# Optimization experiments

Measured on AMD Instinct MI355X. Metric: run time of the kernel, lower is better.

The kernel has to match this reference:

```python
import jax, jax.numpy as jnp
import numpy as np

B, C, N = 4, 512, 4096
C8 = C // 8


def setup_inputs() -> dict:
    key = jax.random.key(0)
    ks = jax.random.split(key, 8)
    s = 0.05  # keep logits in a sane range for softmax
    return {
        "x": jax.random.normal(ks[0], (B, C, N), dtype=jnp.float32),
        "Wq": jax.random.normal(ks[1], (C8, C), dtype=jnp.float32) * s,
        "bq": jax.random.normal(ks[2], (C8,), dtype=jnp.float32) * s,
        "Wk": jax.random.normal(ks[3], (C8, C), dtype=jnp.float32) * s,
        "bk": jax.random.normal(ks[4], (C8,), dtype=jnp.float32) * s,
        "Wv": jax.random.normal(ks[5], (C, C), dtype=jnp.float32) * s,
        "bv": jax.random.normal(ks[6], (C,), dtype=jnp.float32) * s,
        "gamma": jax.random.normal(ks[7], (1,), dtype=jnp.float32),
    }


def reference(x, Wq, bq, Wk, bk, Wv, bv, gamma):
    # Conv1d with kernel_size=1 == per-position linear over channels.
    # x: [B, C, N]
    q = jnp.einsum('oc,bcn->bno', Wq, x) + bq               # [B, N, C8] (already permuted)
    k = jnp.einsum('oc,bcn->bon', Wk, x) + bk[None, :, None]  # [B, C8, N]
    v = jnp.einsum('oc,bcn->bon', Wv, x) + bv[None, :, None]  # [B, C, N]
    # attmap[b, i, j] = <q_i, k_j>; NOTE: no 1/sqrt(d) scaling in the original.
    att = jnp.einsum('bic,bcj->bij', q, k)                  # [B, N, N]
    score = jax.nn.softmax(att, axis=-1)                    # softmax over j
    # out = bmm(value, score.permute(0,2,1)) -> out[b,c,i] = sum_j v[b,c,j] * score[b,i,j]
    out = jnp.einsum('bcj,bij->bci', v, score)              # [B, C, N]
    return gamma * out + x
```

## Files before the change

kernel.cpp:

```cpp
#include <hip/hip_runtime.h>
#include <hip/hip_bf16.h>

typedef __hip_bfloat16 bf16;
typedef __attribute__((ext_vector_type(8))) short short8;
typedef __attribute__((ext_vector_type(4))) float fl4;

#define Bn 4
#define Cn 512
#define C8n 64
#define Nn 4096
#define XKS 536

union BfU { bf16 h; unsigned short u; };
__device__ __forceinline__ unsigned short f2b(float f) { BfU c; c.h = __float2bfloat16(f); return c.u; }
__device__ __forceinline__ float b2f_(unsigned short u) { BfU c; c.u = u; return __bfloat162float(c.h); }

#define MFMA16(a, b, c) __builtin_amdgcn_mfma_f32_16x16x32_bf16(a, b, c, 0, 0, 0)
#define ROR1(x) __uint_as_float(__builtin_amdgcn_update_dpp(0, (int)__float_as_uint(x), 0x121, 0xF, 0xF, true))
#define ROR2(x) __uint_as_float(__builtin_amdgcn_update_dpp(0, (int)__float_as_uint(x), 0x122, 0xF, 0xF, true))
#define ROR4(x) __uint_as_float(__builtin_amdgcn_update_dpp(0, (int)__float_as_uint(x), 0x124, 0xF, 0xF, true))
#define ROR8(x) __uint_as_float(__builtin_amdgcn_update_dpp(0, (int)__float_as_uint(x), 0x128, 0xF, 0xF, true))

__global__ __launch_bounds__(128) void prep_w(
    const float* __restrict__ Wq, const float* __restrict__ bq,
    const float* __restrict__ Wk, const float* __restrict__ bk,
    const float* __restrict__ Wv, const float* __restrict__ bv,
    bf16* __restrict__ whi, bf16* __restrict__ wlo, float* __restrict__ bcat) {
  int row = blockIdx.x;
  int t = threadIdx.x;
  const float* src = (row < 64) ? Wq + (size_t)row * Cn
                   : (row < 128) ? Wk + (size_t)(row - 64) * Cn
                                 : Wv + (size_t)(row - 128) * Cn;
  float4 v = *(const float4*)(src + t * 4);
  unsigned short h0 = f2b(v.x), h1 = f2b(v.y), h2 = f2b(v.z), h3 = f2b(v.w);
  unsigned short l0 = f2b(v.x - b2f_(h0)), l1 = f2b(v.y - b2f_(h1));
  unsigned short l2 = f2b(v.z - b2f_(h2)), l3 = f2b(v.w - b2f_(h3));
  uint2 hu, lu;
  hu.x = h0 | ((unsigned)h1 << 16); hu.y = h2 | ((unsigned)h3 << 16);
  lu.x = l0 | ((unsigned)l1 << 16); lu.y = l2 | ((unsigned)l3 << 16);
  *(uint2*)(whi + (size_t)row * Cn + t * 4) = hu;
  *(uint2*)(wlo + (size_t)row * Cn + t * 4) = lu;
  if (t == 0)
    bcat[row] = (row < 64) ? bq[row] : (row < 128) ? bk[row - 64] : bv[row - 128];
}

__global__ __launch_bounds__(256, 2) void qkv_proj(
    const float* __restrict__ x, const bf16* __restrict__ whi, const bf16* __restrict__ wlo,
    const float* __restrict__ bcat,
    bf16* __restrict__ qhi, bf16* __restrict__ qlo,
    bf16* __restrict__ khi, bf16* __restrict__ klo, bf16* __restrict__ vh) {
  __shared__ bf16 xh[32 * XKS];
  __shared__ bf16 xl[32 * XKS];
  int t = threadIdx.x;
  int b = blockIdx.x >> 7;
  int n0 = (blockIdx.x & 127) << 5;

  const float* xb = x + (size_t)b * Cn * Nn + n0;
  #pragma unroll
  for (int i = 0; i < 8; ++i) {
    int idx = t + i * 256;
    int ng = idx & 7, cp = idx >> 3;
    int c0 = cp * 2;
    float4 va = *(const float4*)(xb + (size_t)c0 * Nn + ng * 4);
    float4 vb2 = *(const float4*)(xb + (size_t)(c0 + 1) * Nn + ng * 4);
    float a_[4] = { va.x, va.y, va.z, va.w };
    float b_[4] = { vb2.x, vb2.y, vb2.z, vb2.w };
    #pragma unroll
    for (int k = 0; k < 4; ++k) {
      int n = ng * 4 + k;
      unsigned short ha = f2b(a_[k]), hb = f2b(b_[k]);
      unsigned short la = f2b(a_[k] - b2f_(ha)), lb = f2b(b_[k] - b2f_(hb));
      *(unsigned*)(&xh[n * XKS + c0]) = (unsigned)ha | ((unsigned)hb << 16);
      *(unsigned*)(&xl[n * XKS + c0]) = (unsigned)la | ((unsigned)lb << 16);
    }
  }

  int w = t >> 6, lane = t & 63, col = lane & 15, quad = lane >> 4;

  fl4 acc[10][2];
  #pragma unroll
  for (int j = 0; j < 10; ++j) {
    int m = (j * 4 + w) * 16 + quad * 4;
    fl4 bi = { bcat[m], bcat[m + 1], bcat[m + 2], bcat[m + 3] };
    acc[j][0] = bi; acc[j][1] = bi;
  }
  __syncthreads();

  for (int kk = 0; kk < 16; ++kk) {
    short8 ah[10], al[10];
    #pragma unroll
    for (int j = 0; j < 10; ++j) {
      size_t off = (size_t)(((j * 4 + w) * 16 + col)) * Cn + kk * 32 + quad * 8;
      ah[j] = *(const short8*)(whi + off);
      al[j] = *(const short8*)(wlo + off);
    }
    short8 bh[2], bl[2];
    #pragma unroll
    for (int ns = 0; ns < 2; ++ns) {
      int o = (ns * 16 + col) * XKS + kk * 32 + quad * 8;
      bh[ns] = *(const short8*)(&xh[o]);
      bl[ns] = *(const short8*)(&xl[o]);
    }
    #pragma unroll
    for (int j = 0; j < 10; ++j) {
      #pragma unroll
      for (int ns = 0; ns < 2; ++ns) {
        acc[j][ns] = MFMA16(ah[j], bh[ns], acc[j][ns]);
        acc[j][ns] = MFMA16(al[j], bh[ns], acc[j][ns]);
        acc[j][ns] = MFMA16(ah[j], bl[ns], acc[j][ns]);
      }
    }
  }

  #pragma unroll
  for (int j = 2; j < 10; ++j) {
    int c = (j * 4 + w) * 16 - 128 + quad * 4;
    #pragma unroll
    for (int ns = 0; ns < 2; ++ns) {
      #pragma unroll
      for (int r = 0; r < 4; ++r) {
        vh[((size_t)b * Cn + c + r) * Nn + n0 + ns * 16 + col] =
            __float2bfloat16(acc[j][ns][r]);
      }
    }
  }

  __syncthreads();
  float* qbuf = (float*)xh;
  float* kbuf = qbuf + 32 * 65;
  {
    int ch = w * 16 + quad * 4;
    #pragma unroll
    for (int ns = 0; ns < 2; ++ns) {
      #pragma unroll
      for (int r = 0; r < 4; ++r) {
        qbuf[(ns * 16 + col) * 65 + ch + r] = acc[0][ns][r];
        kbuf[(ns * 16 + col) * 65 + ch + r] = acc[1][ns][r];
      }
    }
  }
  __syncthreads();
  {
    int n = t >> 3, g = t & 7;
    int och = g * 8;
    size_t orow = ((size_t)b * Nn + n0 + n) * 64 + och;
    float v[8];
    unsigned short h[8], l[8];
    #pragma unroll
    for (int i = 0; i < 8; ++i) v[i] = qbuf[n * 65 + och + i];
    #pragma unroll
    for (int i = 0; i < 8; ++i) { h[i] = f2b(v[i]); l[i] = f2b(v[i] - b2f_(h[i])); }
    uint4 hu, lu;
    hu.x = h[0] | ((unsigned)h[1] << 16); hu.y = h[2] | ((unsigned)h[3] << 16);
    hu.z = h[4] | ((unsigned)h[5] << 16); hu.w = h[6] | ((unsigned)h[7] << 16);
    lu.x = l[0] | ((unsigned)l[1] << 16); lu.y = l[2] | ((unsigned)l[3] << 16);
    lu.z = l[4] | ((unsigned)l[5] << 16); lu.w = l[6] | ((unsigned)l[7] << 16);
    *(uint4*)(qhi + orow) = hu;
    *(uint4*)(qlo + orow) = lu;
    #pragma unroll
    for (int i = 0; i < 8; ++i) v[i] = kbuf[n * 65 + och + i];
    #pragma unroll
    for (int i = 0; i < 8; ++i) { h[i] = f2b(v[i]); l[i] = f2b(v[i] - b2f_(h[i])); }
    hu.x = h[0] | ((unsigned)h[1] << 16); hu.y = h[2] | ((unsigned)h[3] << 16);
    hu.z = h[4] | ((unsigned)h[5] << 16); hu.w = h[6] | ((unsigned)h[7] << 16);
    lu.x = l[0] | ((unsigned)l[1] << 16); lu.y = l[2] | ((unsigned)l[3] << 16);
    lu.z = l[4] | ((unsigned)l[5] << 16); lu.w = l[6] | ((unsigned)l[7] << 16);
    *(uint4*)(khi + orow) = hu;
    *(uint4*)(klo + orow) = lu;
  }
}

__global__ __launch_bounds__(768, 3) void attn(
    const bf16* __restrict__ qhi_g, const bf16* __restrict__ qlo_g,
    const bf16* __restrict__ khi_g, const bf16* __restrict__ klo_g,
    const bf16* __restrict__ vh, const float* __restrict__ x,
    const float* __restrict__ gamma, float* __restrict__ out) {
  __shared__ bf16 kths[2 * 2 * 32 * 72];
  __shared__ bf16 pt[2 * 64 * 40];
  __shared__ float alpha_s[2 * 64];
  __shared__ float lfin[64];

  int t = threadIdx.x;
  int w = t >> 6;
  int lane = t & 63;
  int col = lane & 15;
  int quad = lane >> 4;

  int blk = blockIdx.x;
  int xcd = blk & 7;
  int b = xcd >> 1;
  int itile = ((xcd & 1) << 5) + (blk >> 3);
  int i0 = itile << 6;

  fl4 z = {0.f, 0.f, 0.f, 0.f};

  const bf16* ksrc = (t < 256) ? khi_g : klo_g;
  int hl = (t < 256) ? 0 : 1;
  int ki = t & 255, kj = ki >> 3, koc = ki & 7;
  size_t kgbase = ((size_t)b * Nn + kj) * 64 + koc * 8;
  bf16* kd = kths + hl * 2304 + kj * 72 + koc * 8;
  uint4 kpre;
  if (t < 512) {
    kpre = *(const uint4*)(ksrc + kgbase);
    *(uint4*)kd = kpre;
    kpre = *(const uint4*)(ksrc + kgbase + 32 * 64);
  }

  int it = w;
  short8 qh0, qh1, ql0, ql1;
  float mreg[4], lreg[4];
  if (w < 4) {
    size_t qrow = ((size_t)b * Nn + i0 + it * 16 + col) * 64 + quad * 8;
    qh0 = *(const short8*)(qhi_g + qrow);
    qh1 = *(const short8*)(qhi_g + qrow + 32);
    ql0 = *(const short8*)(qlo_g + qrow);
    ql1 = *(const short8*)(qlo_g + qrow + 32);
    #pragma unroll
    for (int r = 0; r < 4; ++r) { mreg[r] = -3.0e38f; lreg[r] = 0.f; }
  }

  int ow = w - 4, ch0 = ow * 64;
  const bf16* vbase = vh + ((size_t)b * Cn + ch0 + col) * Nn + quad * 8;
  fl4 acc[4][4];
  #pragma unroll
  for (int mt = 0; mt < 4; ++mt)
    #pragma unroll
    for (int nt = 0; nt < 4; ++nt) acc[mt][nt] = z;
  short8 va[4];

  for (int tile = 0; tile < 128; ++tile) {
    __syncthreads();
    int buf = tile & 1;

    if (t < 512) {
      *(uint4*)(kd + (buf ^ 1) * 4608) = kpre;
      int jn = (tile + 2 < 128 ? tile + 2 : 127) << 5;
      kpre = *(const uint4*)(ksrc + kgbase + (size_t)jn * 64);
    }

    if (w < 4) {
      const bf16* kb = kths + buf * 4608;
      const bf16* kbl = kb + 2304;
      short8 khA0 = *(const short8*)(kb + col * 72 + quad * 8);
      short8 khA1 = *(const short8*)(kb + col * 72 + quad * 8 + 32);
      short8 khB0 = *(const short8*)(kb + (16 + col) * 72 + quad * 8);
      short8 khB1 = *(const short8*)(kb + (16 + col) * 72 + quad * 8 + 32);
      short8 klA0 = *(const short8*)(kbl + col * 72 + quad * 8);
      short8 klA1 = *(const short8*)(kbl + col * 72 + quad * 8 + 32);
      short8 klB0 = *(const short8*)(kbl + (16 + col) * 72 + quad * 8);
      short8 klB1 = *(const short8*)(kbl + (16 + col) * 72 + quad * 8 + 32);
      fl4 sA = MFMA16(qh0, khA0, z);
      fl4 sB = MFMA16(qh0, khB0, z);
      sA = MFMA16(qh1, khA1, sA);
      sB = MFMA16(qh1, khB1, sB);
      sA = MFMA16(ql0, khA0, sA);
      sB = MFMA16(ql0, khB0, sB);
      sA = MFMA16(ql1, khA1, sA);
      sB = MFMA16(ql1, khB1, sB);
      sA = MFMA16(qh0, klA0, sA);
      sB = MFMA16(qh0, klB0, sB);
      sA = MFMA16(qh1, klA1, sA);
      sB = MFMA16(qh1, klB1, sB);

      #pragma unroll
      for (int r = 0; r < 4; ++r) {
        float mt_ = fmaxf(sA[r], sB[r]);
        mt_ = fmaxf(mt_, ROR1(mt_)); mt_ = fmaxf(mt_, ROR2(mt_));
        mt_ = fmaxf(mt_, ROR4(mt_)); mt_ = fmaxf(mt_, ROR8(mt_));
        float mnew = fmaxf(mreg[r], mt_);
        float al = __expf(mreg[r] - mnew);
        float pA = __expf(sA[r] - mnew);
        float pB = __expf(sB[r] - mnew);
        float s = pA + pB;
        s += ROR1(s); s += ROR2(s); s += ROR4(s); s += ROR8(s);
        lreg[r] = lreg[r] * al + s;
        mreg[r] = mnew;
        int i = it * 16 + quad * 4 + r;
        pt[buf * 2560 + i * 40 + col] = __float2bfloat16(pA);
        pt[buf * 2560 + i * 40 + 16 + col] = __float2bfloat16(pB);
        if (col == 0) alpha_s[buf * 64 + i] = al;
      }
    } else {
      if (tile > 0) {
        int pb_ = buf ^ 1;
        float av[4];
        #pragma unroll
        for (int nt = 0; nt < 4; ++nt) av[nt] = alpha_s[pb_ * 64 + nt * 16 + col];
        bool nr = (av[0] != 1.f) | (av[1] != 1.f) | (av[2] != 1.f) | (av[3] != 1.f);
        if (__ballot(nr)) {
          #pragma unroll
          for (int mt = 0; mt < 4; ++mt)
            #pragma unroll
            for (int nt = 0; nt < 4; ++nt) acc[mt][nt] *= av[nt];
        }
        short8 pb[4];
        #pragma unroll
        for (int nt = 0; nt < 4; ++nt)
          pb[nt] = *(const short8*)(&pt[pb_ * 2560 + (nt * 16 + col) * 40 + quad * 8]);
        #pragma unroll
        for (int nt = 0; nt < 4; ++nt) {
          acc[0][nt] = MFMA16(va[0], pb[nt], acc[0][nt]);
          acc[1][nt] = MFMA16(va[1], pb[nt], acc[1][nt]);
          acc[2][nt] = MFMA16(va[2], pb[nt], acc[2][nt]);
          acc[3][nt] = MFMA16(va[3], pb[nt], acc[3][nt]);
        }
      }
      const bf16* vj = vbase + (tile << 5);
      va[0] = *(const short8*)(vj);
      va[1] = *(const short8*)(vj + (size_t)16 * Nn);
      va[2] = *(const short8*)(vj + (size_t)32 * Nn);
      va[3] = *(const short8*)(vj + (size_t)48 * Nn);
    }
  }

  if (w < 4 && col == 0) {
    #pragma unroll
    for (int r = 0; r < 4; ++r) lfin[it * 16 + quad * 4 + r] = lreg[r];
  }
  __syncthreads();

  if (w >= 4) {
    float av[4];
    #pragma unroll
    for (int nt = 0; nt < 4; ++nt) av[nt] = alpha_s[64 + nt * 16 + col];
    bool nr = (av[0] != 1.f) | (av[1] != 1.f) | (av[2] != 1.f) | (av[3] != 1.f);
    if (__ballot(nr)) {
      #pragma unroll
      for (int mt = 0; mt < 4; ++mt)
        #pragma unroll
        for (int nt = 0; nt < 4; ++nt) acc[mt][nt] *= av[nt];
    }
    short8 pb[4];
    #pragma unroll
    for (int nt = 0; nt < 4; ++nt)
      pb[nt] = *(const short8*)(&pt[2560 + (nt * 16 + col) * 40 + quad * 8]);
    #pragma unroll
    for (int nt = 0; nt < 4; ++nt) {
      acc[0][nt] = MFMA16(va[0], pb[nt], acc[0][nt]);
      acc[1][nt] = MFMA16(va[1], pb[nt], acc[1][nt]);
      acc[2][nt] = MFMA16(va[2], pb[nt], acc[2][nt]);
      acc[3][nt] = MFMA16(va[3], pb[nt], acc[3][nt]);
    }

    float gm = gamma[0];
    float linv[4];
    #pragma unroll
    for (int nt = 0; nt < 4; ++nt) linv[nt] = 1.f / lfin[nt * 16 + col];
    #pragma unroll
    for (int mt = 0; mt < 4; ++mt) {
      int c = ch0 + mt * 16 + quad * 4;
      #pragma unroll
      for (int r = 0; r < 4; ++r) {
        size_t rowoff = ((size_t)b * Cn + c + r) * Nn + i0;
        #pragma unroll
        for (int nt = 0; nt < 4; ++nt) {
          size_t off = rowoff + nt * 16 + col;
          out[off] = gm * (acc[mt][nt][r] * linv[nt]) + x[off];
        }
      }
    }
  }
}

extern "C" void kernel_launch(void* const* d_in, const int* in_sizes, int n_in,
                              void* d_out, int out_size, void* d_ws, size_t ws_size,
                              hipStream_t stream) {
  const float* x     = (const float*)d_in[0];
  const float* Wq    = (const float*)d_in[1];
  const float* bq    = (const float*)d_in[2];
  const float* Wk    = (const float*)d_in[3];
  const float* bk    = (const float*)d_in[4];
  const float* Wv    = (const float*)d_in[5];
  const float* bv    = (const float*)d_in[6];
  const float* gamma = (const float*)d_in[7];
  float* out = (float*)d_out;

  size_t qkN = (size_t)Bn * Nn * 64;
  bf16* qhi = (bf16*)d_ws;
  bf16* qlo = qhi + qkN;
  bf16* khi = qlo + qkN;
  bf16* klo = khi + qkN;
  bf16* vh  = klo + qkN;
  bf16* whi = vh + (size_t)Bn * Cn * Nn;
  bf16* wlo = whi + (size_t)640 * Cn;
  float* bcat = (float*)(wlo + (size_t)640 * Cn);

  prep_w<<<dim3(640), dim3(128), 0, stream>>>(Wq, bq, Wk, bk, Wv, bv, whi, wlo, bcat);
  qkv_proj<<<dim3(Bn * 128), dim3(256), 0, stream>>>(x, whi, wlo, bcat,
                                                     qhi, qlo, khi, klo, vh);
  attn<<<dim3(256), dim3(768), 0, stream>>>(qhi, qlo, khi, klo, vh, x, gamma, out);
}
```

Baseline: 314.0 us.

## Widen qkv_proj to 512 threads and double-buffer V loads in attention loop

```diff
diff --git a/kernel.cpp b/kernel.cpp
--- a/kernel.cpp
+++ b/kernel.cpp
@@ -44,7 +44,7 @@
     bcat[row] = (row < 64) ? bq[row] : (row < 128) ? bk[row - 64] : bv[row - 128];
 }
 
-__global__ __launch_bounds__(256, 2) void qkv_proj(
+__global__ __launch_bounds__(512, 4) void qkv_proj(
     const float* __restrict__ x, const bf16* __restrict__ whi, const bf16* __restrict__ wlo,
     const float* __restrict__ bcat,
     bf16* __restrict__ qhi, bf16* __restrict__ qlo,
@@ -57,8 +57,8 @@
 
   const float* xb = x + (size_t)b * Cn * Nn + n0;
   #pragma unroll
-  for (int i = 0; i < 8; ++i) {
-    int idx = t + i * 256;
+  for (int i = 0; i < 4; ++i) {
+    int idx = t + i * 512;
     int ng = idx & 7, cp = idx >> 3;
     int c0 = cp * 2;
     float4 va = *(const float4*)(xb + (size_t)c0 * Nn + ng * 4);
@@ -77,20 +77,20 @@
 
   int w = t >> 6, lane = t & 63, col = lane & 15, quad = lane >> 4;
 
-  fl4 acc[10][2];
+  fl4 acc[5][2];
   #pragma unroll
-  for (int j = 0; j < 10; ++j) {
-    int m = (j * 4 + w) * 16 + quad * 4;
+  for (int j = 0; j < 5; ++j) {
+    int m = (j * 8 + w) * 16 + quad * 4;
     fl4 bi = { bcat[m], bcat[m + 1], bcat[m + 2], bcat[m + 3] };
     acc[j][0] = bi; acc[j][1] = bi;
   }
   __syncthreads();
 
   for (int kk = 0; kk < 16; ++kk) {
-    short8 ah[10], al[10];
-    #pragma unroll
-    for (int j = 0; j < 10; ++j) {
-      size_t off = (size_t)(((j * 4 + w) * 16 + col)) * Cn + kk * 32 + quad * 8;
+    short8 ah[5], al[5];
+    #pragma unroll
+    for (int j = 0; j < 5; ++j) {
+      size_t off = (size_t)(((j * 8 + w) * 16 + col)) * Cn + kk * 32 + quad * 8;
       ah[j] = *(const short8*)(whi + off);
       al[j] = *(const short8*)(wlo + off);
     }
@@ -102,7 +102,7 @@
       bl[ns] = *(const short8*)(&xl[o]);
     }
     #pragma unroll
-    for (int j = 0; j < 10; ++j) {
+    for (int j = 0; j < 5; ++j) {
       #pragma unroll
       for (int ns = 0; ns < 2; ++ns) {
         acc[j][ns] = MFMA16(ah[j], bh[ns], acc[j][ns]);
@@ -113,8 +113,8 @@
   }
 
   #pragma unroll
-  for (int j = 2; j < 10; ++j) {
-    int c = (j * 4 + w) * 16 - 128 + quad * 4;
+  for (int j = 1; j < 5; ++j) {
+    int c = (j * 8 + w) * 16 - 128 + quad * 4;
     #pragma unroll
     for (int ns = 0; ns < 2; ++ns) {
       #pragma unroll
@@ -129,46 +129,125 @@
   float* qbuf = (float*)xh;
   float* kbuf = qbuf + 32 * 65;
   {
-    int ch = w * 16 + quad * 4;
+    float* dst = (w < 4) ? qbuf : kbuf;
+    int ch = (w & 3) * 16 + quad * 4;
     #pragma unroll
     for (int ns = 0; ns < 2; ++ns) {
       #pragma unroll
-      for (int r = 0; r < 4; ++r) {
-        qbuf[(ns * 16 + col) * 65 + ch + r] = acc[0][ns][r];
-        kbuf[(ns * 16 + col) * 65 + ch + r] = acc[1][ns][r];
-      }
+      for (int r = 0; r < 4; ++r)
+        dst[(ns * 16 + col) * 65 + ch + r] = acc[0][ns][r];
     }
   }
   __syncthreads();
   {
-    int n = t >> 3, g = t & 7;
-    int och = g * 8;
+    int n = t >> 4, g = t & 15;
+    int och = g * 4;
     size_t orow = ((size_t)b * Nn + n0 + n) * 64 + och;
-    float v[8];
-    unsigned short h[8], l[8];
-    #pragma unroll
-    for (int i = 0; i < 8; ++i) v[i] = qbuf[n * 65 + och + i];
-    #pragma unroll
-    for (int i = 0; i < 8; ++i) { h[i] = f2b(v[i]); l[i] = f2b(v[i] - b2f_(h[i])); }
-    uint4 hu, lu;
+    float v[4];
+    unsigned short h[4], l[4];
+    #pragma unroll
+    for (int i = 0; i < 4; ++i) v[i] = qbuf[n * 65 + och + i];
+    #pragma unroll
+    for (int i = 0; i < 4; ++i) { h[i] = f2b(v[i]); l[i] = f2b(v[i] - b2f_(h[i])); }
+    uint2 hu, lu;
     hu.x = h[0] | ((unsigned)h[1] << 16); hu.y = h[2] | ((unsigned)h[3] << 16);
-    hu.z = h[4] | ((unsigned)h[5] << 16); hu.w = h[6] | ((unsigned)h[7] << 16);
     lu.x = l[0] | ((unsigned)l[1] << 16); lu.y = l[2] | ((unsigned)l[3] << 16);
-    lu.z = l[4] | ((unsigned)l[5] << 16); lu.w = l[6] | ((unsigned)l[7] << 16);
-    *(uint4*)(qhi + orow) = hu;
-    *(uint4*)(qlo + orow) = lu;
-    #pragma unroll
-    for (int i = 0; i < 8; ++i) v[i] = kbuf[n * 65 + och + i];
-    #pragma unroll
-    for (int i = 0; i < 8; ++i) { h[i] = f2b(v[i]); l[i] = f2b(v[i] - b2f_(h[i])); }
+    *(uint2*)(qhi + orow) = hu;
+    *(uint2*)(qlo + orow) = lu;
+    #pragma unroll
+    for (int i = 0; i < 4; ++i) v[i] = kbuf[n * 65 + och + i];
+    #pragma unroll
+    for (int i = 0; i < 4; ++i) { h[i] = f2b(v[i]); l[i] = f2b(v[i] - b2f_(h[i])); }
     hu.x = h[0] | ((unsigned)h[1] << 16); hu.y = h[2] | ((unsigned)h[3] << 16);
-    hu.z = h[4] | ((unsigned)h[5] << 16); hu.w = h[6] | ((unsigned)h[7] << 16);
     lu.x = l[0] | ((unsigned)l[1] << 16); lu.y = l[2] | ((unsigned)l[3] << 16);
-    lu.z = l[4] | ((unsigned)l[5] << 16); lu.w = l[6] | ((unsigned)l[7] << 16);
-    *(uint4*)(khi + orow) = hu;
-    *(uint4*)(klo + orow) = lu;
+    *(uint2*)(khi + orow) = hu;
+    *(uint2*)(klo + orow) = lu;
   }
 }
+
+#define ATTN_ITER(TILE, BUF, VLOAD, VUSE)                                        \
+  {                                                                              \
+    __syncthreads();                                                             \
+    if (t < 512) {                                                               \
+      *(uint4*)(kd + ((BUF) ^ 1) * 4608) = kpre;                                 \
+      int jn = ((TILE) + 2 < 128 ? (TILE) + 2 : 127) << 5;                       \
+      kpre = *(const uint4*)(ksrc + kgbase + (size_t)jn * 64);                   \
+    }                                                                            \
+    if (w < 4) {                                                                 \
+      const bf16* kb = kths + (BUF) * 4608;                                      \
+      const bf16* kbl = kb + 2304;                                               \
+      short8 khA0 = *(const short8*)(kb + col * 72 + quad * 8);                  \
+      short8 khA1 = *(const short8*)(kb + col * 72 + quad * 8 + 32);             \
+      short8 khB0 = *(const short8*)(kb + (16 + col) * 72 + quad * 8);           \
+      short8 khB1 = *(const short8*)(kb + (16 + col) * 72 + quad * 8 + 32);      \
+      short8 klA0 = *(const short8*)(kbl + col * 72 + quad * 8);                 \
+      short8 klA1 = *(const short8*)(kbl + col * 72 + quad * 8 + 32);            \
+      short8 klB0 = *(const short8*)(kbl + (16 + col) * 72 + quad * 8);          \
+      short8 klB1 = *(const short8*)(kbl + (16 + col) * 72 + quad * 8 + 32);     \
+      fl4 c1 = MFMA16(qh0, khA0, z);                                             \
+      fl4 c2 = MFMA16(ql0, khA0, z);                                             \
+      fl4 c3 = MFMA16(qh0, klA0, z);                                             \
+      fl4 d1 = MFMA16(qh0, khB0, z);                                             \
+      fl4 d2 = MFMA16(ql0, khB0, z);                                             \
+      fl4 d3 = MFMA16(qh0, klB0, z);                                             \
+      c1 = MFMA16(qh1, khA1, c1);                                                \
+      c2 = MFMA16(ql1, khA1, c2);                                                \
+      c3 = MFMA16(qh1, klA1, c3);                                                \
+      d1 = MFMA16(qh1, khB1, d1);                                                \
+      d2 = MFMA16(ql1, khB1, d2);                                                \
+      d3 = MFMA16(qh1, klB1, d3);                                                \
+      fl4 sA = (c1 + c2) + c3;                                                   \
+      fl4 sB = (d1 + d2) + d3;                                                   \
+      _Pragma("unroll")                                                          \
+      for (int r = 0; r < 4; ++r) {                                              \
+        float mt_ = fmaxf(sA[r], sB[r]);                                         \
+        mt_ = fmaxf(mt_, ROR1(mt_)); mt_ = fmaxf(mt_, ROR2(mt_));                \
+        mt_ = fmaxf(mt_, ROR4(mt_)); mt_ = fmaxf(mt_, ROR8(mt_));                \
+        float mnew = fmaxf(mreg[r], mt_);                                        \
+        float al = __expf(mreg[r] - mnew);                                       \
+        float pA = __expf(sA[r] - mnew);                                         \
+        float pB = __expf(sB[r] - mnew);                                         \
+        float s = pA + pB;                                                       \
+        s += ROR1(s); s += ROR2(s); s += ROR4(s); s += ROR8(s);                  \
+        lreg[r] = lreg[r] * al + s;                                              \
+        mreg[r] = mnew;                                                          \
+        int i = it * 16 + quad * 4 + r;                                          \
+        pt[(BUF) * 2560 + i * 40 + col] = __float2bfloat16(pA);                  \
+        pt[(BUF) * 2560 + i * 40 + 16 + col] = __float2bfloat16(pB);             \
+        if (col == 0) alpha_s[(BUF) * 64 + i] = al;                              \
+      }                                                                          \
+    } else {                                                                     \
+      const bf16* vj = vbase + ((TILE) << 5);                                    \
+      VLOAD[0] = *(const short8*)(vj);                                           \
+      VLOAD[1] = *(const short8*)(vj + (size_t)16 * Nn);                         \
+      VLOAD[2] = *(const short8*)(vj + (size_t)32 * Nn);                         \
+      VLOAD[3] = *(const short8*)(vj + (size_t)48 * Nn);                         \
+      if ((TILE) > 0) {                                                          \
+        int pb_ = (BUF) ^ 1;                                                     \
+        float av[4];                                                             \
+        _Pragma("unroll")                                                        \
+        for (int nt = 0; nt < 4; ++nt) av[nt] = alpha_s[pb_ * 64 + nt * 16 + col]; \
+        bool nr = (av[0] != 1.f) | (av[1] != 1.f) | (av[2] != 1.f) | (av[3] != 1.f); \
+        if (__ballot(nr)) {                                                      \
+          _Pragma("unroll")                                                      \
+          for (int mt = 0; mt < 4; ++mt)                                         \
+            _Pragma("unroll")                                                    \
+            for (int nt = 0; nt < 4; ++nt) acc[mt][nt] *= av[nt];                \
+        }                                                                        \
+        short8 pb[4];                                                            \
+        _Pragma("unroll")                                                        \
+        for (int nt = 0; nt < 4; ++nt)                                           \
+          pb[nt] = *(const short8*)(&pt[pb_ * 2560 + (nt * 16 + col) * 40 + quad * 8]); \
+        _Pragma("unroll")                                                        \
+        for (int nt = 0; nt < 4; ++nt) {                                         \
+          acc[0][nt] = MFMA16(VUSE[0], pb[nt], acc[0][nt]);                      \
+          acc[1][nt] = MFMA16(VUSE[1], pb[nt], acc[1][nt]);                      \
+          acc[2][nt] = MFMA16(VUSE[2], pb[nt], acc[2][nt]);                      \
+          acc[3][nt] = MFMA16(VUSE[3], pb[nt], acc[3][nt]);                      \
+        }                                                                        \
+      }                                                                          \
+    }                                                                            \
+  }
 
 __global__ __launch_bounds__(768, 3) void attn(
     const bf16* __restrict__ qhi_g, const bf16* __restrict__ qlo_g,
@@ -226,91 +305,11 @@
   for (int mt = 0; mt < 4; ++mt)
     #pragma unroll
     for (int nt = 0; nt < 4; ++nt) acc[mt][nt] = z;
-  short8 va[4];
-
-  for (int tile = 0; tile < 128; ++tile) {
-    __syncthreads();
-    int buf = tile & 1;
-
-    if (t < 512) {
-      *(uint4*)(kd + (buf ^ 1) * 4608) = kpre;
-      int jn = (tile + 2 < 128 ? tile + 2 : 127) << 5;
-      kpre = *(const uint4*)(ksrc + kgbase + (size_t)jn * 64);
-    }
-
-    if (w < 4) {
-      const bf16* kb = kths + buf * 4608;
-      const bf16* kbl = kb + 2304;
-      short8 khA0 = *(const short8*)(kb + col * 72 + quad * 8);
-      short8 khA1 = *(const short8*)(kb + col * 72 + quad * 8 + 32);
-      short8 khB0 = *(const short8*)(kb + (16 + col) * 72 + quad * 8);
-      short8 khB1 = *(const short8*)(kb + (16 + col) * 72 + quad * 8 + 32);
-      short8 klA0 = *(const short8*)(kbl + col * 72 + quad * 8);
-      short8 klA1 = *(const short8*)(kbl + col * 72 + quad * 8 + 32);
-      short8 klB0 = *(const short8*)(kbl + (16 + col) * 72 + quad * 8);
-      short8 klB1 = *(const short8*)(kbl + (16 + col) * 72 + quad * 8 + 32);
-      fl4 sA = MFMA16(qh0, khA0, z);
-      fl4 sB = MFMA16(qh0, khB0, z);
-      sA = MFMA16(qh1, khA1, sA);
-      sB = MFMA16(qh1, khB1, sB);
-      sA = MFMA16(ql0, khA0, sA);
-      sB = MFMA16(ql0, khB0, sB);
-      sA = MFMA16(ql1, khA1, sA);
-      sB = MFMA16(ql1, khB1, sB);
-      sA = MFMA16(qh0, klA0, sA);
-      sB = MFMA16(qh0, klB0, sB);
-      sA = MFMA16(qh1, klA1, sA);
-      sB = MFMA16(qh1, klB1, sB);
-
-      #pragma unroll
-      for (int r = 0; r < 4; ++r) {
-        float mt_ = fmaxf(sA[r], sB[r]);
-        mt_ = fmaxf(mt_, ROR1(mt_)); mt_ = fmaxf(mt_, ROR2(mt_));
-        mt_ = fmaxf(mt_, ROR4(mt_)); mt_ = fmaxf(mt_, ROR8(mt_));
-        float mnew = fmaxf(mreg[r], mt_);
-        float al = __expf(mreg[r] - mnew);
-        float pA = __expf(sA[r] - mnew);
-        float pB = __expf(sB[r] - mnew);
-        float s = pA + pB;
-        s += ROR1(s); s += ROR2(s); s += ROR4(s); s += ROR8(s);
-        lreg[r] = lreg[r] * al + s;
-        mreg[r] = mnew;
-        int i = it * 16 + quad * 4 + r;
-        pt[buf * 2560 + i * 40 + col] = __float2bfloat16(pA);
-        pt[buf * 2560 + i * 40 + 16 + col] = __float2bfloat16(pB);
-        if (col == 0) alpha_s[buf * 64 + i] = al;
-      }
-    } else {
-      if (tile > 0) {
-        int pb_ = buf ^ 1;
-        float av[4];
-        #pragma unroll
-        for (int nt = 0; nt < 4; ++nt) av[nt] = alpha_s[pb_ * 64 + nt * 16 + col];
-        bool nr = (av[0] != 1.f) | (av[1] != 1.f) | (av[2] != 1.f) | (av[3] != 1.f);
-        if (__ballot(nr)) {
-          #pragma unroll
-          for (int mt = 0; mt < 4; ++mt)
-            #pragma unroll
-            for (int nt = 0; nt < 4; ++nt) acc[mt][nt] *= av[nt];
-        }
-        short8 pb[4];
-        #pragma unroll
-        for (int nt = 0; nt < 4; ++nt)
-          pb[nt] = *(const short8*)(&pt[pb_ * 2560 + (nt * 16 + col) * 40 + quad * 8]);
-        #pragma unroll
-        for (int nt = 0; nt < 4; ++nt) {
-          acc[0][nt] = MFMA16(va[0], pb[nt], acc[0][nt]);
-          acc[1][nt] = MFMA16(va[1], pb[nt], acc[1][nt]);
-          acc[2][nt] = MFMA16(va[2], pb[nt], acc[2][nt]);
-          acc[3][nt] = MFMA16(va[3], pb[nt], acc[3][nt]);
-        }
-      }
-      const bf16* vj = vbase + (tile << 5);
-      va[0] = *(const short8*)(vj);
-      va[1] = *(const short8*)(vj + (size_t)16 * Nn);
-      va[2] = *(const short8*)(vj + (size_t)32 * Nn);
-      va[3] = *(const short8*)(vj + (size_t)48 * Nn);
-    }
+  short8 vaA[4], vaB[4];
+
+  for (int tp = 0; tp < 64; ++tp) {
+    ATTN_ITER(tp * 2, 0, vaA, vaB)
+    ATTN_ITER(tp * 2 + 1, 1, vaB, vaA)
   }
 
   if (w < 4 && col == 0) {
@@ -336,10 +335,10 @@
       pb[nt] = *(const short8*)(&pt[2560 + (nt * 16 + col) * 40 + quad * 8]);
     #pragma unroll
     for (int nt = 0; nt < 4; ++nt) {
-      acc[0][nt] = MFMA16(va[0], pb[nt], acc[0][nt]);
-      acc[1][nt] = MFMA16(va[1], pb[nt], acc[1][nt]);
-      acc[2][nt] = MFMA16(va[2], pb[nt], acc[2][nt]);
-      acc[3][nt] = MFMA16(va[3], pb[nt], acc[3][nt]);
+      acc[0][nt] = MFMA16(vaB[0], pb[nt], acc[0][nt]);
+      acc[1][nt] = MFMA16(vaB[1], pb[nt], acc[1][nt]);
+      acc[2][nt] = MFMA16(vaB[2], pb[nt], acc[2][nt]);
+      acc[3][nt] = MFMA16(vaB[3], pb[nt], acc[3][nt]);
     }
 
     float gm = gamma[0];
@@ -386,7 +385,7 @@
   float* bcat = (float*)(wlo + (size_t)640 * Cn);
 
   prep_w<<<dim3(640), dim3(128), 0, stream>>>(Wq, bq, Wk, bk, Wv, bv, whi, wlo, bcat);
-  qkv_proj<<<dim3(Bn * 128), dim3(256), 0, stream>>>(x, whi, wlo, bcat,
+  qkv_proj<<<dim3(Bn * 128), dim3(512), 0, stream>>>(x, whi, wlo, bcat,
                                                      qhi, qlo, khi, klo, vh);
   attn<<<dim3(256), dim3(768), 0, stream>>>(qhi, qlo, khi, klo, vh, x, gamma, out);
 }
```

Measured after the change: 442.6 us. 41.0% more time.

## Split x transpose into prep kernel and tile QKV projection as async-LDS GEMM

Applied to the files above, without the earlier changes.

```diff
diff --git a/kernel.cpp b/kernel.cpp
--- a/kernel.cpp
+++ b/kernel.cpp
@@ -9,7 +9,6 @@
 #define Cn 512
 #define C8n 64
 #define Nn 4096
-#define XKS 536
 
 union BfU { bf16 h; unsigned short u; };
 __device__ __forceinline__ unsigned short f2b(float f) { BfU c; c.h = __float2bfloat16(f); return c.u; }
@@ -20,6 +19,10 @@
 #define ROR2(x) __uint_as_float(__builtin_amdgcn_update_dpp(0, (int)__float_as_uint(x), 0x122, 0xF, 0xF, true))
 #define ROR4(x) __uint_as_float(__builtin_amdgcn_update_dpp(0, (int)__float_as_uint(x), 0x124, 0xF, 0xF, true))
 #define ROR8(x) __uint_as_float(__builtin_amdgcn_update_dpp(0, (int)__float_as_uint(x), 0x128, 0xF, 0xF, true))
+
+typedef const __attribute__((address_space(1))) char* gas1_t;
+typedef __attribute__((address_space(3))) char* las3_t;
+#define GL16(gp, lp) __builtin_amdgcn_global_load_lds((gas1_t)(gp), (las3_t)(lp), 16, 0, 0)
 
 __global__ __launch_bounds__(128) void prep_w(
     const float* __restrict__ Wq, const float* __restrict__ bq,
@@ -44,130 +47,177 @@
     bcat[row] = (row < 64) ? bq[row] : (row < 128) ? bk[row - 64] : bv[row - 128];
 }
 
-__global__ __launch_bounds__(256, 2) void qkv_proj(
-    const float* __restrict__ x, const bf16* __restrict__ whi, const bf16* __restrict__ wlo,
-    const float* __restrict__ bcat,
+__global__ __launch_bounds__(256) void prep_x(
+    const float* __restrict__ x, bf16* __restrict__ xth, bf16* __restrict__ xtl) {
+  __shared__ float ts[32][33];
+  int t = threadIdx.x;
+  int gid = blockIdx.x;
+  int b = gid >> 11;
+  int rem = gid & 2047;
+  int ct = rem >> 7, nt = rem & 127;
+  int c0 = ct << 5, n0 = nt << 5;
+  {
+    int cl = t >> 3, nf = t & 7;
+    float4 v = *(const float4*)(x + ((size_t)b * Cn + c0 + cl) * Nn + n0 + nf * 4);
+    ts[cl][nf * 4 + 0] = v.x; ts[cl][nf * 4 + 1] = v.y;
+    ts[cl][nf * 4 + 2] = v.z; ts[cl][nf * 4 + 3] = v.w;
+  }
+  __syncthreads();
+  {
+    int nl = t >> 3, cg = t & 7;
+    float a0 = ts[cg * 4 + 0][nl], a1 = ts[cg * 4 + 1][nl];
+    float a2 = ts[cg * 4 + 2][nl], a3 = ts[cg * 4 + 3][nl];
+    unsigned short h0 = f2b(a0), h1 = f2b(a1), h2 = f2b(a2), h3 = f2b(a3);
+    unsigned short l0 = f2b(a0 - b2f_(h0)), l1 = f2b(a1 - b2f_(h1));
+    unsigned short l2 = f2b(a2 - b2f_(h2)), l3 = f2b(a3 - b2f_(h3));
+    uint2 hu, lu;
+    hu.x = h0 | ((unsigned)h1 << 16); hu.y = h2 | ((unsigned)h3 << 16);
+    lu.x = l0 | ((unsigned)l1 << 16); lu.y = l2 | ((unsigned)l3 << 16);
+    size_t off = ((size_t)b * Nn + n0 + nl) * Cn + c0 + cg * 4;
+    *(uint2*)(xth + off) = hu;
+    *(uint2*)(xtl + off) = lu;
+  }
+}
+
+__global__ __launch_bounds__(256, 3) void qkv_gemm(
+    const bf16* __restrict__ whi, const float* __restrict__ bcat,
+    const bf16* __restrict__ xth,
     bf16* __restrict__ qhi, bf16* __restrict__ qlo,
     bf16* __restrict__ khi, bf16* __restrict__ klo, bf16* __restrict__ vh) {
-  __shared__ bf16 xh[32 * XKS];
-  __shared__ bf16 xl[32 * XKS];
+  __shared__ char smem[32768];
   int t = threadIdx.x;
-  int b = blockIdx.x >> 7;
-  int n0 = (blockIdx.x & 127) << 5;
-
-  const float* xb = x + (size_t)b * Cn * Nn + n0;
+  int w = t >> 6, lane = t & 63, col = lane & 15, quad = lane >> 4;
+  int wm = w & 1, wn = w >> 1;
+
+  int gid = blockIdx.x;
+  int b = gid / 160;
+  int r2 = gid - b * 160;
+  int mb = r2 >> 5;
+  int nb = r2 & 31;
+  int m0 = mb << 7, n0 = nb << 7;
+
+  const char* wB = (const char*)whi;
+  const char* xB = (const char*)xth;
+  size_t aRow0 = ((size_t)(m0 + lane)) * 1024 + w * 16;
+  size_t aRow1 = ((size_t)(m0 + 64 + lane)) * 1024 + w * 16;
+  size_t bRow0 = ((size_t)b * Nn + n0 + lane) * 1024 + w * 16;
+  size_t bRow1 = bRow0 + (size_t)64 * 1024;
+  const size_t WLO_OFF = (size_t)640 * 1024;
+  const size_t XTL_OFF = (size_t)Bn * Nn * 1024;
+
+  #define STAGE(G, BUF)                                                        \
+    {                                                                          \
+      int p_ = (G) >> 4;                                                       \
+      size_t ka_ = (size_t)((G) & 15) * 64 + (p_ == 2 ? WLO_OFF : 0);          \
+      size_t kb_ = (size_t)((G) & 15) * 64 + (p_ == 1 ? XTL_OFF : 0);          \
+      char* L_ = smem + (BUF) * 16384;                                         \
+      GL16(wB + aRow0 + ka_, L_ + w * 2048);                                   \
+      GL16(wB + aRow1 + ka_, L_ + w * 2048 + 1024);                            \
+      GL16(xB + bRow0 + kb_, L_ + 8192 + w * 2048);                            \
+      GL16(xB + bRow1 + kb_, L_ + 8192 + w * 2048 + 1024);                     \
+    }
+
+  fl4 z = {0.f, 0.f, 0.f, 0.f};
+  fl4 acc[4][4];
   #pragma unroll
-  for (int i = 0; i < 8; ++i) {
-    int idx = t + i * 256;
-    int ng = idx & 7, cp = idx >> 3;
-    int c0 = cp * 2;
-    float4 va = *(const float4*)(xb + (size_t)c0 * Nn + ng * 4);
-    float4 vb2 = *(const float4*)(xb + (size_t)(c0 + 1) * Nn + ng * 4);
-    float a_[4] = { va.x, va.y, va.z, va.w };
-    float b_[4] = { vb2.x, vb2.y, vb2.z, vb2.w };
-    #pragma unroll
-    for (int k = 0; k < 4; ++k) {
-      int n = ng * 4 + k;
-      unsigned short ha = f2b(a_[k]), hb = f2b(b_[k]);
-      unsigned short la = f2b(a_[k] - b2f_(ha)), lb = f2b(b_[k] - b2f_(hb));
-      *(unsigned*)(&xh[n * XKS + c0]) = (unsigned)ha | ((unsigned)hb << 16);
-      *(unsigned*)(&xl[n * XKS + c0]) = (unsigned)la | ((unsigned)lb << 16);
-    }
-  }
-
-  int w = t >> 6, lane = t & 63, col = lane & 15, quad = lane >> 4;
-
-  fl4 acc[10][2];
+  for (int mt = 0; mt < 4; ++mt)
+    #pragma unroll
+    for (int nt = 0; nt < 4; ++nt) acc[mt][nt] = z;
+
+  STAGE(0, 0)
+  for (int g = 0; g < 48; ++g) {
+    __syncthreads();
+    if (g < 47) STAGE(g + 1, (g + 1) & 1)
+    const bf16* L = (const bf16*)(smem + (g & 1) * 16384);
+    const bf16* Ab = L;
+    const bf16* Bb = L + 4096;
+    short8 af[4], bfr[4];
+    #pragma unroll
+    for (int mt = 0; mt < 4; ++mt)
+      af[mt] = *(const short8*)(Ab + quad * 1024 + (wm * 64 + mt * 16 + col) * 8);
+    #pragma unroll
+    for (int nt = 0; nt < 4; ++nt)
+      bfr[nt] = *(const short8*)(Bb + quad * 1024 + (wn * 64 + nt * 16 + col) * 8);
+    #pragma unroll
+    for (int mt = 0; mt < 4; ++mt)
+      #pragma unroll
+      for (int nt = 0; nt < 4; ++nt)
+        acc[mt][nt] = MFMA16(af[mt], bfr[nt], acc[mt][nt]);
+  }
+  __syncthreads();
+
   #pragma unroll
-  for (int j = 0; j < 10; ++j) {
-    int m = (j * 4 + w) * 16 + quad * 4;
-    fl4 bi = { bcat[m], bcat[m + 1], bcat[m + 2], bcat[m + 3] };
-    acc[j][0] = bi; acc[j][1] = bi;
-  }
-  __syncthreads();
-
-  for (int kk = 0; kk < 16; ++kk) {
-    short8 ah[10], al[10];
-    #pragma unroll
-    for (int j = 0; j < 10; ++j) {
-      size_t off = (size_t)(((j * 4 + w) * 16 + col)) * Cn + kk * 32 + quad * 8;
-      ah[j] = *(const short8*)(whi + off);
-      al[j] = *(const short8*)(wlo + off);
-    }
-    short8 bh[2], bl[2];
-    #pragma unroll
-    for (int ns = 0; ns < 2; ++ns) {
-      int o = (ns * 16 + col) * XKS + kk * 32 + quad * 8;
-      bh[ns] = *(const short8*)(&xh[o]);
-      bl[ns] = *(const short8*)(&xl[o]);
-    }
-    #pragma unroll
-    for (int j = 0; j < 10; ++j) {
-      #pragma unroll
-      for (int ns = 0; ns < 2; ++ns) {
-        acc[j][ns] = MFMA16(ah[j], bh[ns], acc[j][ns]);
-        acc[j][ns] = MFMA16(al[j], bh[ns], acc[j][ns]);
-        acc[j][ns] = MFMA16(ah[j], bl[ns], acc[j][ns]);
-      }
-    }
-  }
-
-  #pragma unroll
-  for (int j = 2; j < 10; ++j) {
-    int c = (j * 4 + w) * 16 - 128 + quad * 4;
-    #pragma unroll
-    for (int ns = 0; ns < 2; ++ns) {
+  for (int mt = 0; mt < 4; ++mt)
+    #pragma unroll
+    for (int r = 0; r < 4; ++r) {
+      float bb = bcat[m0 + wm * 64 + mt * 16 + quad * 4 + r];
+      #pragma unroll
+      for (int nt = 0; nt < 4; ++nt) acc[mt][nt][r] += bb;
+    }
+
+  if (mb > 0) {
+    #pragma unroll
+    for (int mt = 0; mt < 4; ++mt)
       #pragma unroll
       for (int r = 0; r < 4; ++r) {
-        vh[((size_t)b * Cn + c + r) * Nn + n0 + ns * 16 + col] =
-            __float2bfloat16(acc[j][ns][r]);
-      }
-    }
-  }
-
-  __syncthreads();
-  float* qbuf = (float*)xh;
-  float* kbuf = qbuf + 32 * 65;
-  {
-    int ch = w * 16 + quad * 4;
-    #pragma unroll
-    for (int ns = 0; ns < 2; ++ns) {
-      #pragma unroll
-      for (int r = 0; r < 4; ++r) {
-        qbuf[(ns * 16 + col) * 65 + ch + r] = acc[0][ns][r];
-        kbuf[(ns * 16 + col) * 65 + ch + r] = acc[1][ns][r];
-      }
-    }
-  }
-  __syncthreads();
-  {
-    int n = t >> 3, g = t & 7;
-    int och = g * 8;
-    size_t orow = ((size_t)b * Nn + n0 + n) * 64 + och;
-    float v[8];
-    unsigned short h[8], l[8];
-    #pragma unroll
-    for (int i = 0; i < 8; ++i) v[i] = qbuf[n * 65 + och + i];
-    #pragma unroll
-    for (int i = 0; i < 8; ++i) { h[i] = f2b(v[i]); l[i] = f2b(v[i] - b2f_(h[i])); }
-    uint4 hu, lu;
-    hu.x = h[0] | ((unsigned)h[1] << 16); hu.y = h[2] | ((unsigned)h[3] << 16);
-    hu.z = h[4] | ((unsigned)h[5] << 16); hu.w = h[6] | ((unsigned)h[7] << 16);
-    lu.x = l[0] | ((unsigned)l[1] << 16); lu.y = l[2] | ((unsigned)l[3] << 16);
-    lu.z = l[4] | ((unsigned)l[5] << 16); lu.w = l[6] | ((unsigned)l[7] << 16);
-    *(uint4*)(qhi + orow) = hu;
-    *(uint4*)(qlo + orow) = lu;
-    #pragma unroll
-    for (int i = 0; i < 8; ++i) v[i] = kbuf[n * 65 + och + i];
-    #pragma unroll
-    for (int i = 0; i < 8; ++i) { h[i] = f2b(v[i]); l[i] = f2b(v[i] - b2f_(h[i])); }
-    hu.x = h[0] | ((unsigned)h[1] << 16); hu.y = h[2] | ((unsigned)h[3] << 16);
-    hu.z = h[4] | ((unsigned)h[5] << 16); hu.w = h[6] | ((unsigned)h[7] << 16);
-    lu.x = l[0] | ((unsigned)l[1] << 16); lu.y = l[2] | ((unsigned)l[3] << 16);
-    lu.z = l[4] | ((unsigned)l[5] << 16); lu.w = l[6] | ((unsigned)l[7] << 16);
-    *(uint4*)(khi + orow) = hu;
-    *(uint4*)(klo + orow) = lu;
-  }
+        int c = m0 - 128 + wm * 64 + mt * 16 + quad * 4 + r;
+        size_t rowo = ((size_t)b * Cn + c) * Nn + n0;
+        #pragma unroll
+        for (int nt = 0; nt < 4; ++nt)
+          vh[rowo + wn * 64 + nt * 16 + col] = __float2bfloat16(acc[mt][nt][r]);
+      }
+  } else {
+    float* trs = (float*)smem;
+    #pragma unroll
+    for (int p4 = 0; p4 < 4; ++p4) {
+      if (wn == (p4 >> 1)) {
+        #pragma unroll
+        for (int ntl = 0; ntl < 2; ++ntl) {
+          int nt = (p4 & 1) * 2 + ntl;
+          int nl = ntl * 16 + col;
+          #pragma unroll
+          for (int mt = 0; mt < 4; ++mt)
+            #pragma unroll
+            for (int r = 0; r < 4; ++r)
+              trs[nl * 132 + wm * 64 + mt * 16 + quad * 4 + r] = acc[mt][nt][r];
+        }
+      }
+      __syncthreads();
+      {
+        int nl = t >> 3, seg = t & 7;
+        float v[16];
+        #pragma unroll
+        for (int i = 0; i < 16; ++i) v[i] = trs[nl * 132 + seg * 16 + i];
+        unsigned short h[16], l[16];
+        #pragma unroll
+        for (int i = 0; i < 16; ++i) { h[i] = f2b(v[i]); l[i] = f2b(v[i] - b2f_(h[i])); }
+        uint4 hu0, hu1, lu0, lu1;
+        hu0.x = h[0] | ((unsigned)h[1] << 16);  hu0.y = h[2] | ((unsigned)h[3] << 16);
+        hu0.z = h[4] | ((unsigned)h[5] << 16);  hu0.w = h[6] | ((unsigned)h[7] << 16);
+        hu1.x = h[8] | ((unsigned)h[9] << 16);  hu1.y = h[10] | ((unsigned)h[11] << 16);
+        hu1.z = h[12] | ((unsigned)h[13] << 16); hu1.w = h[14] | ((unsigned)h[15] << 16);
+        lu0.x = l[0] | ((unsigned)l[1] << 16);  lu0.y = l[2] | ((unsigned)l[3] << 16);
+        lu0.z = l[4] | ((unsigned)l[5] << 16);  lu0.w = l[6] | ((unsigned)l[7] << 16);
+        lu1.x = l[8] | ((unsigned)l[9] << 16);  lu1.y = l[10] | ((unsigned)l[11] << 16);
+        lu1.z = l[12] | ((unsigned)l[13] << 16); lu1.w = l[14] | ((unsigned)l[15] << 16);
+        int n = n0 + p4 * 32 + nl;
+        size_t base = ((size_t)b * Nn + n) * 64;
+        if (seg < 4) {
+          *(uint4*)(qhi + base + seg * 16) = hu0;
+          *(uint4*)(qhi + base + seg * 16 + 8) = hu1;
+          *(uint4*)(qlo + base + seg * 16) = lu0;
+          *(uint4*)(qlo + base + seg * 16 + 8) = lu1;
+        } else {
+          *(uint4*)(khi + base + (seg - 4) * 16) = hu0;
+          *(uint4*)(khi + base + (seg - 4) * 16 + 8) = hu1;
+          *(uint4*)(klo + base + (seg - 4) * 16) = lu0;
+          *(uint4*)(klo + base + (seg - 4) * 16 + 8) = lu1;
+        }
+      }
+      __syncthreads();
+    }
+  }
+  #undef STAGE
 }
 
 __global__ __launch_bounds__(768, 3) void attn(
@@ -249,18 +299,20 @@
       short8 klA1 = *(const short8*)(kbl + col * 72 + quad * 8 + 32);
       short8 klB0 = *(const short8*)(kbl + (16 + col) * 72 + quad * 8);
       short8 klB1 = *(const short8*)(kbl + (16 + col) * 72 + quad * 8 + 32);
-      fl4 sA = MFMA16(qh0, khA0, z);
-      fl4 sB = MFMA16(qh0, khB0, z);
-      sA = MFMA16(qh1, khA1, sA);
-      sB = MFMA16(qh1, khB1, sB);
-      sA = MFMA16(ql0, khA0, sA);
-      sB = MFMA16(ql0, khB0, sB);
-      sA = MFMA16(ql1, khA1, sA);
-      sB = MFMA16(ql1, khB1, sB);
-      sA = MFMA16(qh0, klA0, sA);
-      sB = MFMA16(qh0, klB0, sB);
-      sA = MFMA16(qh1, klA1, sA);
-      sB = MFMA16(qh1, klB1, sB);
+      fl4 s0 = MFMA16(qh0, khA0, z);
+      fl4 s1 = MFMA16(qh0, khB0, z);
+      s0 = MFMA16(qh1, khA1, s0);
+      s1 = MFMA16(qh1, khB1, s1);
+      s0 = MFMA16(ql0, khA0, s0);
+      s1 = MFMA16(ql0, khB0, s1);
+      s0 = MFMA16(ql1, khA1, s0);
+      s1 = MFMA16(ql1, khB1, s1);
+      s0 = MFMA16(qh0, klA0, s0);
+      s1 = MFMA16(qh0, klB0, s1);
+      s0 = MFMA16(qh1, klA1, s0);
+      s1 = MFMA16(qh1, klB1, s1);
+      fl4 sA = s0;
+      fl4 sB = s1;
 
       #pragma unroll
       for (int r = 0; r < 4; ++r) {
@@ -385,8 +437,12 @@
   bf16* wlo = whi + (size_t)640 * Cn;
   float* bcat = (float*)(wlo + (size_t)640 * Cn);
 
+  bf16* xth = (bf16*)d_out;
+  bf16* xtl = xth + (size_t)Bn * Nn * Cn;
+
   prep_w<<<dim3(640), dim3(128), 0, stream>>>(Wq, bq, Wk, bk, Wv, bv, whi, wlo, bcat);
-  qkv_proj<<<dim3(Bn * 128), dim3(256), 0, stream>>>(x, whi, wlo, bcat,
-                                                     qhi, qlo, khi, klo, vh);
+  prep_x<<<dim3(8192), dim3(256), 0, stream>>>(x, xth, xtl);
+  qkv_gemm<<<dim3(640), dim3(256), 0, stream>>>(whi, bcat, xth,
+                                                qhi, qlo, khi, klo, vh);
   attn<<<dim3(256), dim3(768), 0, stream>>>(qhi, qlo, khi, klo, vh, x, gamma, out);
 }
```

Measured after the change: 312.0 us. Within noise of the previous version (-0.6%).
